# Optimization experiments

Hardware: AMD Instinct MI355X
Metric: run time of the kernel (lower is better)

## Reference

```python
import jax, jax.numpy as jnp
import numpy as np

EPS = 1e-8  # torch CosineSimilarity default eps


def setup_inputs() -> dict:
    key = jax.random.key(0)
    k1, k2, k3, k4, k5, k6, k7, k8 = jax.random.split(key, 8)
    N1, N2 = 8192, 8192
    # first 3 cols: geometric features; col 3: integer class label stored as float
    e1_feat = jax.random.normal(k1, (N1, 3), dtype=jnp.float32)
    e2_feat = jax.random.normal(k2, (N2, 3), dtype=jnp.float32)
    e1_cls = jax.random.randint(k3, (N1, 1), 0, 8).astype(jnp.float32)
    e2_cls = jax.random.randint(k4, (N2, 1), 0, 8).astype(jnp.float32)
    edges1 = jnp.concatenate([e1_feat, e1_cls], axis=-1)
    edges2 = jnp.concatenate([e2_feat, e2_cls], axis=-1)
    W1 = jax.random.normal(k5, (3, 64), dtype=jnp.float32) * 0.5
    b1 = jax.random.normal(k6, (64,), dtype=jnp.float32) * 0.1
    W2 = jax.random.normal(k7, (64, 32), dtype=jnp.float32) * 0.1
    b2 = jax.random.normal(k8, (32,), dtype=jnp.float32) * 0.1
    return {"edges1": edges1, "edges2": edges2, "W1": W1, "b1": b1, "W2": W2, "b2": b2}


def _branch(x, W1, b1, W2, b2):
    h = jax.nn.relu(x @ W1 + b1)
    return h @ W2 + b2  # [N, 32]


def reference(edges1, edges2, W1, b1, W2, b2):
    f1 = _branch(edges1[:, :3], W1, b1, W2, b2)  # [N1, 32]
    f2 = _branch(edges2[:, :3], W1, b1, W2, b2)  # [N2, 32]
    # pairwise cosine similarity without materializing [N1, N2, 32]
    dots = jnp.einsum('id,jd->ij', f1, f2)                  # [N1, N2]
    n1 = jnp.linalg.norm(f1, axis=-1)                        # [N1]
    n2 = jnp.linalg.norm(f2, axis=-1)                        # [N2]
    denom = jnp.maximum(n1[:, None] * n2[None, :], EPS)
    dist_mat = dots / denom                                  # [N1, N2]
    # pairwise label-equality mask (all label columns must match)
    cls1 = edges1[:, 3:].astype(jnp.int32)                   # [N1, C]
    cls2 = edges2[:, 3:].astype(jnp.int32)                   # [N2, C]
    cls_aff = jnp.all(cls1[:, None, :] == cls2[None, :, :], axis=-1)  # [N1, N2] bool
    return cls_aff.astype(dist_mat.dtype) * dist_mat
```

## Files before the change

### kernel.cpp

```cpp
#include <hip/hip_runtime.h>


typedef __bf16 bf16x8 __attribute__((ext_vector_type(8)));
typedef float floatx4 __attribute__((ext_vector_type(4)));

__global__ __launch_bounds__(64) void mlp_norm_kernel(
    const float* __restrict__ e1, const float* __restrict__ e2,
    const float* __restrict__ W1, const float* __restrict__ b1,
    const float* __restrict__ W2, const float* __restrict__ b2,
    __bf16* __restrict__ f1b, __bf16* __restrict__ f2b,
    int* __restrict__ cls1, int* __restrict__ cls2, int N1, int N2)
{
    __shared__ __align__(16) float sW1[192];
    __shared__ float sb1[64];
    __shared__ __align__(16) float sW2[2048];
    __shared__ float sb2[32];
    for (int i = threadIdx.x; i < 192; i += 64) sW1[i] = W1[i];
    sb1[threadIdx.x] = b1[threadIdx.x];
    for (int i = threadIdx.x; i < 2048; i += 64) sW2[i] = W2[i];
    if (threadIdx.x < 32) sb2[threadIdx.x] = b2[threadIdx.x];
    __syncthreads();

    int t = blockIdx.x * 64 + threadIdx.x;
    if (t >= N1 + N2) return;

    const float* src;
    __bf16* fout;
    int* cout;
    int row;
    if (t < N1) { row = t;      src = e1 + (size_t)row * 4; fout = f1b; cout = cls1; }
    else        { row = t - N1; src = e2 + (size_t)row * 4; fout = f2b; cout = cls2; }

    float x0 = src[0], x1 = src[1], x2 = src[2];
    int lbl = (int)src[3];

    float f[32];
#pragma unroll
    for (int k = 0; k < 32; ++k) f[k] = sb2[k];

#pragma unroll 4
    for (int j = 0; j < 64; ++j) {
        float h = fmaf(x0, sW1[j], fmaf(x1, sW1[64 + j], fmaf(x2, sW1[128 + j], sb1[j])));
        h = fmaxf(h, 0.0f);
        const floatx4* w2 = (const floatx4*)(sW2 + j * 32);
#pragma unroll
        for (int k4 = 0; k4 < 8; ++k4) {
            floatx4 w = w2[k4];
            f[k4 * 4 + 0] = fmaf(h, w[0], f[k4 * 4 + 0]);
            f[k4 * 4 + 1] = fmaf(h, w[1], f[k4 * 4 + 1]);
            f[k4 * 4 + 2] = fmaf(h, w[2], f[k4 * 4 + 2]);
            f[k4 * 4 + 3] = fmaf(h, w[3], f[k4 * 4 + 3]);
        }
    }

    float ss = 0.0f;
#pragma unroll
    for (int k = 0; k < 32; ++k) ss = fmaf(f[k], f[k], ss);
    float n = sqrtf(ss);
    float scale = (n > 1e-20f) ? (1.0f / n) : 0.0f;

    __bf16* dst = fout + (size_t)row * 32;
#pragma unroll
    for (int k = 0; k < 32; ++k) dst[k] = (__bf16)(f[k] * scale);
    cout[row] = lbl;
}

#define TROW 520
__global__ __launch_bounds__(256) void pair_cos_kernel(
    const __bf16* __restrict__ f1b, const __bf16* __restrict__ f2b,
    const int* __restrict__ cls1, const int* __restrict__ cls2,
    float* __restrict__ out, int N2, int ncg)
{
    __shared__ __align__(16) float tile[16 * TROW];

    const int lane = threadIdx.x & 63;
    const int w = threadIdx.x >> 6;
    const int istrip = blockIdx.x / ncg;
    const int cg = blockIdx.x - istrip * ncg;
    const int i0 = istrip * 16;
    const int j0 = cg * 512;
    const int r16 = lane & 15;
    const int q = lane >> 4;

    bf16x8 bfrag = *(const bf16x8*)(f1b + (size_t)(i0 + r16) * 32 + q * 8);
    const int c1 = cls1[i0 + r16];

#pragma unroll
    for (int t = 0; t < 8; ++t) {
        const int jc = w * 128 + t * 16;
        const int j = j0 + jc;
        bf16x8 afrag = *(const bf16x8*)(f2b + (size_t)(j + r16) * 32 + q * 8);
        int4 c2 = *(const int4*)(cls2 + j + q * 4);

        floatx4 acc = {0.0f, 0.0f, 0.0f, 0.0f};
        floatx4 d = __builtin_amdgcn_mfma_f32_16x16x32_bf16(afrag, bfrag, acc, 0, 0, 0);

        floatx4 m;
        m[0] = (c2.x == c1) ? d[0] : 0.0f;
        m[1] = (c2.y == c1) ? d[1] : 0.0f;
        m[2] = (c2.z == c1) ? d[2] : 0.0f;
        m[3] = (c2.w == c1) ? d[3] : 0.0f;
        *(floatx4*)(tile + r16 * TROW + jc + q * 4) = m;
    }

    __syncthreads();

    const int r = threadIdx.x >> 7;
    const int cb = (threadIdx.x & 127) << 2;
    const size_t obase = (size_t)i0 * N2 + j0 + cb;
#pragma unroll
    for (int rr0 = 0; rr0 < 16; rr0 += 2) {
        const int rr = rr0 + r;
        floatx4 v = *(const floatx4*)(tile + rr * TROW + cb);
        __builtin_nontemporal_store(v, (floatx4*)(out + obase + (size_t)rr * N2));
    }
}

extern "C" void kernel_launch(void* const* d_in, const int* in_sizes, int n_in,
                              void* d_out, int out_size, void* d_ws, size_t ws_size,
                              hipStream_t stream) {
    const float* e1 = (const float*)d_in[0];
    const float* e2 = (const float*)d_in[1];
    const float* W1 = (const float*)d_in[2];
    const float* b1 = (const float*)d_in[3];
    const float* W2 = (const float*)d_in[4];
    const float* b2 = (const float*)d_in[5];
    float* out = (float*)d_out;

    const int N1 = in_sizes[0] / 4;
    const int N2 = in_sizes[1] / 4;

    char* ws = (char*)d_ws;
    __bf16* f1b = (__bf16*)ws;
    __bf16* f2b = (__bf16*)(ws + (size_t)N1 * 64);
    int* cls1 = (int*)(ws + (size_t)(N1 + N2) * 64);
    int* cls2 = cls1 + N1;

    int nrows = N1 + N2;
    mlp_norm_kernel<<<(nrows + 63) / 64, 64, 0, stream>>>(
        e1, e2, W1, b1, W2, b2, f1b, f2b, cls1, cls2, N1, N2);

    int ncg = N2 / 512;
    int nblocks = (N1 / 16) * ncg;
    pair_cos_kernel<<<nblocks, 256, 0, stream>>>(
        f1b, f2b, cls1, cls2, out, N2, ncg);
}
```

Measured before the change: 287.3 us.

## Use per-wave LDS tiles, drop block barrier, use plain stores, vectorize bf16 writes

The pair kernel now gives each wave its own 16x128 LDS tile, so the block-wide __syncthreads is replaced by a wave-local lgkmcnt wait. Each wave writes out its own 128-column slab, which gives 512-byte row segments instead of 2KB ones. Nontemporal stores become regular stores, and the launch bounds ask for 4 blocks per CU. The MLP kernel packs its bf16 output into 16-byte vector stores. Shorter contiguous write segments and dropping the nontemporal hint could hurt write efficiency on the 256MB output.

```diff
diff --git a/kernel.cpp b/kernel.cpp
--- a/kernel.cpp
+++ b/kernel.cpp
@@ -61,34 +61,39 @@
 
     __bf16* dst = fout + (size_t)row * 32;
 #pragma unroll
-    for (int k = 0; k < 32; ++k) dst[k] = (__bf16)(f[k] * scale);
+    for (int k8 = 0; k8 < 4; ++k8) {
+        bf16x8 o;
+#pragma unroll
+        for (int k = 0; k < 8; ++k) o[k] = (__bf16)(f[k8 * 8 + k] * scale);
+        *(bf16x8*)(dst + k8 * 8) = o;
+    }
     cout[row] = lbl;
 }
 
-#define TROW 520
-__global__ __launch_bounds__(256) void pair_cos_kernel(
+#define SW 136
+__global__ __launch_bounds__(256, 4) void pair_cos_kernel(
     const __bf16* __restrict__ f1b, const __bf16* __restrict__ f2b,
     const int* __restrict__ cls1, const int* __restrict__ cls2,
     float* __restrict__ out, int N2, int ncg)
 {
-    __shared__ __align__(16) float tile[16 * TROW];
+    __shared__ __align__(16) float tile[4][16 * SW];
 
     const int lane = threadIdx.x & 63;
     const int w = threadIdx.x >> 6;
     const int istrip = blockIdx.x / ncg;
     const int cg = blockIdx.x - istrip * ncg;
     const int i0 = istrip * 16;
-    const int j0 = cg * 512;
+    const int j0w = cg * 512 + w * 128;
     const int r16 = lane & 15;
     const int q = lane >> 4;
 
     bf16x8 bfrag = *(const bf16x8*)(f1b + (size_t)(i0 + r16) * 32 + q * 8);
     const int c1 = cls1[i0 + r16];
+    float* tw = &tile[w][0];
 
 #pragma unroll
     for (int t = 0; t < 8; ++t) {
-        const int jc = w * 128 + t * 16;
-        const int j = j0 + jc;
+        const int j = j0w + t * 16;
         bf16x8 afrag = *(const bf16x8*)(f2b + (size_t)(j + r16) * 32 + q * 8);
         int4 c2 = *(const int4*)(cls2 + j + q * 4);
 
@@ -100,19 +105,19 @@
         m[1] = (c2.y == c1) ? d[1] : 0.0f;
         m[2] = (c2.z == c1) ? d[2] : 0.0f;
         m[3] = (c2.w == c1) ? d[3] : 0.0f;
-        *(floatx4*)(tile + r16 * TROW + jc + q * 4) = m;
+        *(floatx4*)(tw + r16 * SW + t * 16 + q * 4) = m;
     }
 
-    __syncthreads();
+    asm volatile("s_waitcnt lgkmcnt(0)" ::: "memory");
 
-    const int r = threadIdx.x >> 7;
-    const int cb = (threadIdx.x & 127) << 2;
-    const size_t obase = (size_t)i0 * N2 + j0 + cb;
+    const int rh = lane >> 5;
+    const int c4 = (lane & 31) << 2;
+    const size_t obase = (size_t)i0 * N2 + j0w + c4;
 #pragma unroll
-    for (int rr0 = 0; rr0 < 16; rr0 += 2) {
-        const int rr = rr0 + r;
-        floatx4 v = *(const floatx4*)(tile + rr * TROW + cb);
-        __builtin_nontemporal_store(v, (floatx4*)(out + obase + (size_t)rr * N2));
+    for (int it = 0; it < 8; ++it) {
+        const int r = it * 2 + rh;
+        floatx4 v = *(const floatx4*)(tw + r * SW + c4);
+        *(floatx4*)(out + obase + (size_t)r * N2) = v;
     }
 }
 
```

New measurement: 277.4 us. 1.04x faster.
